# Kernel optimization log

Measured on AMD Instinct MI355X. Metric: run time of the kernel, lower is better.

The kernel has to match this reference:

```python
import jax, jax.numpy as jnp
import numpy as np
from jax import lax

HS, WS = 8, 8  # pattern_size


def setup_inputs() -> dict:
    key = jax.random.key(0)
    k1, k2, k3 = jax.random.split(key, 3)
    B, C, T, H, W = 2, 64, 16, 112, 112
    Cout, K = 64, 3
    x = jax.random.normal(k1, (B, C, T, H, W), dtype=jnp.float32)
    # one independent Conv3d weight/bias per (h, w) phase in the 8x8 pattern
    weight = jax.random.normal(k2, (HS, WS, Cout, C, K, K, K), dtype=jnp.float32) * 0.05
    bias = jax.random.normal(k3, (HS, WS, Cout), dtype=jnp.float32) * 0.05
    return {"x": x, "weight": weight, "bias": bias}


def reference(x, weight, bias):
    hs, ws = HS, WS
    B, C, T, H, W = x.shape
    Cout = weight.shape[2]
    # torch F.pad(x, (hs-1, hs-1, ws-1, ws-1, 1, 1)): W padded by hs-1, H by ws-1, T by 1
    paded = jnp.pad(x, ((0, 0), (0, 0), (1, 1), (ws - 1, ws - 1), (hs - 1, hs - 1)))
    Ho, Wo = H // hs, W // ws  # conv output spatial size per phase: (H-3)//8 + 1 = H//8
    rows = []
    for h in range(hs):
        cols = []
        for w in range(ws):
            sl = paded[:, :, :, h:H + h, w:W + w]  # [B, C, T+2, H, W]
            y = lax.conv_general_dilated(
                sl, weight[h, w],
                window_strides=(1, hs, ws), padding='VALID',
                dimension_numbers=('NCDHW', 'OIDHW', 'NCDHW'))  # [B, Cout, T, Ho, Wo]
            cols.append(y + bias[h, w][None, :, None, None, None])
        rows.append(jnp.stack(cols, 0))
    res = jnp.stack(rows, 0)  # [hs, ws, B, Cout, T, Ho, Wo]
    # out[:, :, :, h + hs*i, w + ws*j] = res[h, w, :, :, :, i, j]
    out = jnp.transpose(res, (2, 3, 4, 5, 0, 6, 1))  # [B, Cout, T, Ho, hs, Wo, ws]
    return out.reshape(B, Cout, T, H, W)
```

## Files before the change

### kernel.cpp

```cpp
#include <hip/hip_runtime.h>
#include <hip/hip_bf16.h>
#include <stdint.h>

typedef __attribute__((ext_vector_type(8))) short short8;
typedef __attribute__((ext_vector_type(4))) float f32x4;

#define WPP_BYTES 14155776ull
#define XPP_BYTES 66355200ull

__device__ __forceinline__ void gl2lds16(const void* g, void* l) {
    __builtin_amdgcn_global_load_lds(
        (const __attribute__((address_space(1))) unsigned int*)g,
        (__attribute__((address_space(3))) unsigned int*)l, 16, 0, 0);
}

__global__ __launch_bounds__(256)
void bzero(uint4* __restrict__ xpp) {
    const uint4 z = {0u, 0u, 0u, 0u};
    const int total = 935936;
    for (int idx = blockIdx.x * 256 + threadIdx.x; idx < total;
         idx += gridDim.x * 256) {
        int u;
        if (idx < 276480) {
            int slab = idx / 2160, off = idx % 2160;
            u = slab * 32400 + off;
        } else if (idx < 534528) {
            int k = idx - 276480;
            int run = k / 144, off = k % 144;
            int slab = run / 14, rho = run % 14 + 1;
            u = slab * 32400 + rho * 2160 + off;
        } else {
            int k = idx - 534528;
            int run = k / 8, off = k % 8;
            int slab = run / 392, r2 = run % 392;
            int rho = r2 / 28 + 1, r3 = r2 % 28;
            int cwo = r3 / 2 + 1, d = (r3 & 1) * 17;
            u = slab * 32400 + rho * 2160 + cwo * 144 + d * 8 + off;
        }
        xpp[u] = z;
    }
}

__global__ __launch_bounds__(512)
void xform_x(const float* __restrict__ xin, __hip_bfloat16* __restrict__ xpp) {
    extern __shared__ __hip_bfloat16 Xl[];
    const int bid = blockIdx.x;
    const int rho = bid % 14, d = (bid / 14) % 16, b = bid / 224;
    const int tid = threadIdx.x;
    for (int f = tid; f < 64 * 8 * 28; f += 512) {
        int ci = f / 224, rem = f % 224;
        int r = rem / 28, c4 = (rem % 28) * 4;
        const float4 v = *(const float4*)&xin[
            ((((size_t)b * 64 + ci) * 16 + d) * 112 + (rho * 8 + r)) * 112 + c4];
        const float vv[4] = {v.x, v.y, v.z, v.w};
#pragma unroll
        for (int u = 0; u < 4; ++u) {
            int c = c4 + u;
            Xl[(r * 112 + c) * 64 + (ci ^ ((c & 7) << 3))] = __float2bfloat16(vv[u]);
        }
    }
    __syncthreads();
    for (int f = tid; f < 896 * 8; f += 512) {
        int pos = f >> 3, j = f & 7;
        int r = pos / 112, c = pos % 112;
        int cw = c & 7, cwo = c >> 3;
        uint4 v = *(const uint4*)&Xl[pos * 64 + ((j * 8) ^ ((c & 7) << 3))];
        size_t dst = (((((size_t)(r * 8 + cw) * 2 + b) * 15 + (rho + 1)) * 15
                       + (cwo + 1)) * 18 + (d + 1)) * 64 + j * 8;
        *(uint4*)(xpp + dst) = v;
    }
}

__global__ __launch_bounds__(256)
void xform_w(const float* __restrict__ wt, __hip_bfloat16* __restrict__ wpp) {
    __shared__ __hip_bfloat16 lw[8 * 27 * 72];
    const int hw = blockIdx.x >> 3, cc = blockIdx.x & 7;
    for (int f = threadIdx.x; f < 8 * 64 * 27; f += 256) {
        int k = f % 27, ci = (f / 27) % 64, co = f / (27 * 64);
        float v = wt[(size_t)hw * 110592 + (size_t)(cc * 8 + co) * 1728 + ci * 27 + k];
        lw[(co * 27 + k) * 72 + ci] = __float2bfloat16(v);
    }
    __syncthreads();
    for (int f = threadIdx.x; f < 27 * 8 * 8; f += 256) {
        int cic = f % 8, co = (f / 8) % 8, k = f / 64;
        uint4 v = *(const uint4*)&lw[(co * 27 + k) * 72 + cic * 8];
        size_t dst = (((size_t)hw * 27 + k) * 64 + (cc * 8 + co)) * 64 + cic * 8;
        *(uint4*)(wpp + dst) = v;
    }
}


__global__ __launch_bounds__(256, 2)
void patgemm(const __hip_bfloat16* __restrict__ xpp,
             const char* __restrict__ wppc,
             const float* __restrict__ bs,
             float* __restrict__ out) {
    extern __shared__ char smem[];
    const char* xppc = (const char*)xpp;
    const int bid = blockIdx.x;
    const int h = bid & 7, w = (bid >> 3) & 7, b = (bid >> 6) & 1, mc = bid >> 7;
    const int hw = h * 8 + w;
    const int tid = threadIdx.x, wv = tid >> 6;
    const int lane = tid & 63, col = lane & 15, quad = lane >> 4;
    const int mg = wv >> 1, ng = wv & 1;

    uint32_t aoff[4];
#pragma unroll
    for (int i = 0; i < 4; ++i) {
        int u = tid + i * 256; if (u > 1007) u = 1007;
        int wo = u / 72, rem = u - wo * 72;
        int d = rem >> 2, qp = rem & 3, q = qp ^ ((d >> 1) & 3);
        aoff[i] = (uint32_t)(wo * 2304 + d * 128 + q * 16);
    }
    uint32_t boff[2];
#pragma unroll
    for (int i = 0; i < 2; ++i) {
        int u = tid + i * 256;
        boff[i] = (uint32_t)((u >> 3) * 128 + (((u & 7) ^ ((u >> 3) & 7)) << 4));
    }
    uint32_t rofs[3];
#pragma unroll
    for (int kd = 0; kd < 3; ++kd) {
        int d = col + kd;
        rofs[kd] = (uint32_t)(d * 64 + ((quad ^ ((d >> 1) & 3)) << 4));
    }
    uint32_t bofsw[2];
#pragma unroll
    for (int hf = 0; hf < 2; ++hf)
        bofsw[hf] = (uint32_t)(col * 128 + (((hf * 4 + quad) ^ (col & 7)) << 4));

    f32x4 acc[7][2];
#pragma unroll
    for (int j = 0; j < 7; ++j)
#pragma unroll
        for (int n = 0; n < 2; ++n) acc[j][n] = (f32x4){0.f, 0.f, 0.f, 0.f};

    const char* wbase = wppc + (size_t)hw * 221184;

    auto lineBase = [&](int p) -> const char* {
        const int kh = (p >= 6) ? 2 : (p >= 3 ? 1 : 0);
        const int kw = p - 3 * kh;
        const int r0 = h + kh - 7, c0 = w + kw - 7;
        return xppc + (size_t)(((((r0 & 7) * 8 + (c0 & 7)) * 2 + b) * 15
                    + ((r0 >> 3) + 1 + mc)) * 15 + ((c0 >> 3) + 1)) * 2304;
    };
    auto STGA = [&](const char* lb, int hf, int buf) {
#pragma unroll
        for (int i = 0; i < 4; ++i)
            gl2lds16(lb + aoff[i] + hf * 64,
                     smem + buf * 16384 + (tid + i * 256) * 16);
    };
    auto STGB = [&](int tap, int slot) {
#pragma unroll
        for (int i = 0; i < 2; ++i)
            gl2lds16(wbase + (size_t)tap * 8192 + boff[i],
                     smem + 32768 + slot * 8192 + (tid + i * 256) * 16);
    };

    const char* lb = lineBase(0);
    STGA(lb, 0, 0);
    STGB(0, 0); STGB(9, 1); STGB(18, 2);
    __syncthreads();

#pragma unroll 1
    for (int p = 0; p < 9; ++p) {
        const int pp = p & 1;
        STGA(lb, 1, 1);
        if (p < 8) {
            const int sb = (1 - pp) * 3;
            STGB(p + 1, sb); STGB(p + 10, sb + 1); STGB(p + 19, sb + 2);
        }
#pragma unroll
        for (int kd = 0; kd < 3; ++kd) {
            const char* Bb = smem + 32768 + (pp * 3 + kd) * 8192;
            short8 bf0 = *(const short8*)(Bb + (ng * 2 + 0) * 2048 + bofsw[0]);
            short8 bf1 = *(const short8*)(Bb + (ng * 2 + 1) * 2048 + bofsw[0]);
#pragma unroll
            for (int j = 0; j < 7; ++j) {
                short8 af = *(const short8*)(smem + (mg * 7 + j) * 1152 + rofs[kd]);
                acc[j][0] = __builtin_amdgcn_mfma_f32_16x16x32_bf16(af, bf0, acc[j][0], 0, 0, 0);
                acc[j][1] = __builtin_amdgcn_mfma_f32_16x16x32_bf16(af, bf1, acc[j][1], 0, 0, 0);
            }
        }
        __syncthreads();
        if (p < 8) { lb = lineBase(p + 1); STGA(lb, 0, 0); }
#pragma unroll
        for (int kd = 0; kd < 3; ++kd) {
            const char* Bb = smem + 32768 + (pp * 3 + kd) * 8192;
            short8 bf0 = *(const short8*)(Bb + (ng * 2 + 0) * 2048 + bofsw[1]);
            short8 bf1 = *(const short8*)(Bb + (ng * 2 + 1) * 2048 + bofsw[1]);
#pragma unroll
            for (int j = 0; j < 7; ++j) {
                short8 af = *(const short8*)(smem + 16384 + (mg * 7 + j) * 1152 + rofs[kd]);
                acc[j][0] = __builtin_amdgcn_mfma_f32_16x16x32_bf16(af, bf0, acc[j][0], 0, 0, 0);
                acc[j][1] = __builtin_amdgcn_mfma_f32_16x16x32_bf16(af, bf1, acc[j][1], 0, 0, 0);
            }
        }
        __syncthreads();
    }

    const float* bsl = bs + hw * 64;
    const int y = 8 * mc + h;
#pragma unroll
    for (int j = 0; j < 7; ++j) {
        const int x = 8 * (mg * 7 + j) + w;
#pragma unroll
        for (int n = 0; n < 2; ++n) {
            const int co = (ng * 2 + n) * 16 + col;
            const float bv = bsl[co];
#pragma unroll
            for (int jj = 0; jj < 4; ++jj) {
                const int t = quad * 4 + jj;
                out[((((size_t)b * 64 + co) * 16 + t) * 112 + y) * 112 + x]
                    = acc[j][n][jj] + bv;
            }
        }
    }
}

#define XL_ROWSTRIDE 116
#define WL_WSTRIDE (17*27)

__global__ __launch_bounds__(256, 3)
void patconv3d_fp32(const float* __restrict__ xin,
                    const float* __restrict__ wt,
                    const float* __restrict__ bs,
                    float* __restrict__ out) {
    __shared__ float Xl[3*3*7*XL_ROWSTRIDE];
    __shared__ float Wl[8*WL_WSTRIDE];
    const int bid = blockIdx.x;
    const int ct = bid & 3, hb = (bid >> 2) & 1, h = (bid >> 3) & 7;
    const int t = (bid >> 6) & 15, b = (bid >> 10) & 1;
    const int tid = threadIdx.x;
    const int xl = tid & 127, cg = tid >> 7;
    const int xr = (xl < 112) ? xl : 111;
    const int wq = xl & 7;
    float acc[8][7];
#pragma unroll
    for (int c = 0; c < 8; ++c)
#pragma unroll
        for (int ho = 0; ho < 7; ++ho) acc[c][ho] = 0.f;
    for (int ci = 0; ci < 64; ++ci) {
        __syncthreads();
        for (int idx = tid; idx < 3 * 3 * 7 * 114; idx += 256) {
            int c = idx % 114, rest = idx / 114;
            int ho = rest % 7; rest /= 7;
            int kh = rest % 3, kd = rest / 3;
            int r = 8 * (hb * 7 + ho) + h + kh - 7;
            int d = t + kd - 1, colx = c - 7;
            float v = 0.f;
            if (r >= 0 && d >= 0 && d < 16 && colx >= 0)
                v = xin[(((size_t)(b * 64 + ci) * 16 + d) * 112 + r) * 112 + colx];
            Xl[((kd * 3 + kh) * 7 + ho) * XL_ROWSTRIDE + c] = v;
        }
        for (int idx = tid; idx < 8 * 16 * 27; idx += 256) {
            int k2 = idx % 27, rest = idx / 27;
            int co_l = rest % 16, wi = rest / 16;
            Wl[wi * WL_WSTRIDE + co_l * 27 + k2] =
                wt[(((size_t)(h * 8 + wi) * 64 + (ct * 16 + co_l)) * 64 + ci) * 27 + k2];
        }
        __syncthreads();
#pragma unroll
        for (int kd = 0; kd < 3; ++kd)
#pragma unroll
            for (int kh = 0; kh < 3; ++kh)
#pragma unroll
                for (int kw = 0; kw < 3; ++kw) {
                    const int k2 = (kd * 3 + kh) * 3 + kw;
                    float xv[7];
#pragma unroll
                    for (int ho = 0; ho < 7; ++ho)
                        xv[ho] = Xl[((kd * 3 + kh) * 7 + ho) * XL_ROWSTRIDE + xr + kw];
                    float wv[8];
#pragma unroll
                    for (int c = 0; c < 8; ++c)
                        wv[c] = Wl[wq * WL_WSTRIDE + (cg * 8 + c) * 27 + k2];
#pragma unroll
                    for (int c = 0; c < 8; ++c)
#pragma unroll
                        for (int ho = 0; ho < 7; ++ho)
                            acc[c][ho] += wv[c] * xv[ho];
                }
    }
    if (xl < 112) {
#pragma unroll
        for (int c = 0; c < 8; ++c) {
            const int co = ct * 16 + cg * 8 + c;
            const float bv = bs[(h * 8 + wq) * 64 + co];
#pragma unroll
            for (int ho = 0; ho < 7; ++ho) {
                const int y = 8 * (hb * 7 + ho) + h;
                out[(((size_t)(b * 64 + co) * 16 + t) * 112 + y) * 112 + xl] = acc[c][ho] + bv;
            }
        }
    }
}

extern "C" void kernel_launch(void* const* d_in, const int* in_sizes, int n_in,
                              void* d_out, int out_size, void* d_ws, size_t ws_size,
                              hipStream_t stream) {
    const float* x  = (const float*)d_in[0];
    const float* wg = (const float*)d_in[1];
    const float* bi = (const float*)d_in[2];
    float* out = (float*)d_out;
    if (ws_size >= WPP_BYTES + XPP_BYTES) {
        __hip_bfloat16* wpp = (__hip_bfloat16*)d_ws;
        __hip_bfloat16* xpp = (__hip_bfloat16*)((char*)d_ws + WPP_BYTES);
        bzero<<<1024, 256, 0, stream>>>((uint4*)xpp);
        xform_x<<<448, 512, 114688, stream>>>(x, xpp);
        xform_w<<<512, 256, 0, stream>>>(wg, wpp);
        patgemm<<<1792, 256, 81920, stream>>>(xpp, (const char*)wpp, bi, out);
    } else {
        patconv3d_fp32<<<2048, 256, 0, stream>>>(x, wg, bi, out);
    }
}
```

Before: 255.8 us.

## Merge prep kernels into one launch; load weights directly to registers

Merges the zero-fill, input transform and weight transform kernels into a single launch, with block-index ranges picking the role, to remove launch gaps. In the GEMM kernel the weight fragments are now loaded from global memory straight into registers each tap instead of being staged in LDS. This shrinks LDS use to 32 KB per block and raises the occupancy hint from 2 to 4 blocks per CU. The cost is more register pressure from twelve held fragments, and weight global loads that are no longer double-buffered and may stall the MFMA loop.

Result: slower. 379.8 us (+48.5%).

```diff
diff --git a/kernel.cpp b/kernel.cpp
--- a/kernel.cpp
+++ b/kernel.cpp
@@ -14,88 +14,87 @@
         (__attribute__((address_space(3))) unsigned int*)l, 16, 0, 0);
 }
 
-__global__ __launch_bounds__(256)
-void bzero(uint4* __restrict__ xpp) {
-    const uint4 z = {0u, 0u, 0u, 0u};
-    const int total = 935936;
-    for (int idx = blockIdx.x * 256 + threadIdx.x; idx < total;
-         idx += gridDim.x * 256) {
-        int u;
-        if (idx < 276480) {
-            int slab = idx / 2160, off = idx % 2160;
-            u = slab * 32400 + off;
-        } else if (idx < 534528) {
-            int k = idx - 276480;
-            int run = k / 144, off = k % 144;
-            int slab = run / 14, rho = run % 14 + 1;
-            u = slab * 32400 + rho * 2160 + off;
-        } else {
-            int k = idx - 534528;
-            int run = k / 8, off = k % 8;
-            int slab = run / 392, r2 = run % 392;
-            int rho = r2 / 28 + 1, r3 = r2 % 28;
-            int cwo = r3 / 2 + 1, d = (r3 & 1) * 17;
-            u = slab * 32400 + rho * 2160 + cwo * 144 + d * 8 + off;
-        }
-        xpp[u] = z;
-    }
-}
-
 __global__ __launch_bounds__(512)
-void xform_x(const float* __restrict__ xin, __hip_bfloat16* __restrict__ xpp) {
-    extern __shared__ __hip_bfloat16 Xl[];
+void prep(const float* __restrict__ xin, const float* __restrict__ wt,
+          __hip_bfloat16* __restrict__ xpp, __hip_bfloat16* __restrict__ wpp) {
+    extern __shared__ char smc[];
     const int bid = blockIdx.x;
-    const int rho = bid % 14, d = (bid / 14) % 16, b = bid / 224;
     const int tid = threadIdx.x;
-    for (int f = tid; f < 64 * 8 * 28; f += 512) {
-        int ci = f / 224, rem = f % 224;
-        int r = rem / 28, c4 = (rem % 28) * 4;
-        const float4 v = *(const float4*)&xin[
-            ((((size_t)b * 64 + ci) * 16 + d) * 112 + (rho * 8 + r)) * 112 + c4];
-        const float vv[4] = {v.x, v.y, v.z, v.w};
-#pragma unroll
-        for (int u = 0; u < 4; ++u) {
-            int c = c4 + u;
-            Xl[(r * 112 + c) * 64 + (ci ^ ((c & 7) << 3))] = __float2bfloat16(vv[u]);
-        }
-    }
-    __syncthreads();
-    for (int f = tid; f < 896 * 8; f += 512) {
-        int pos = f >> 3, j = f & 7;
-        int r = pos / 112, c = pos % 112;
-        int cw = c & 7, cwo = c >> 3;
-        uint4 v = *(const uint4*)&Xl[pos * 64 + ((j * 8) ^ ((c & 7) << 3))];
-        size_t dst = (((((size_t)(r * 8 + cw) * 2 + b) * 15 + (rho + 1)) * 15
-                       + (cwo + 1)) * 18 + (d + 1)) * 64 + j * 8;
-        *(uint4*)(xpp + dst) = v;
-    }
-}
-
-__global__ __launch_bounds__(256)
-void xform_w(const float* __restrict__ wt, __hip_bfloat16* __restrict__ wpp) {
-    __shared__ __hip_bfloat16 lw[8 * 27 * 72];
-    const int hw = blockIdx.x >> 3, cc = blockIdx.x & 7;
-    for (int f = threadIdx.x; f < 8 * 64 * 27; f += 256) {
-        int k = f % 27, ci = (f / 27) % 64, co = f / (27 * 64);
-        float v = wt[(size_t)hw * 110592 + (size_t)(cc * 8 + co) * 1728 + ci * 27 + k];
-        lw[(co * 27 + k) * 72 + ci] = __float2bfloat16(v);
-    }
-    __syncthreads();
-    for (int f = threadIdx.x; f < 27 * 8 * 8; f += 256) {
-        int cic = f % 8, co = (f / 8) % 8, k = f / 64;
-        uint4 v = *(const uint4*)&lw[(co * 27 + k) * 72 + cic * 8];
-        size_t dst = (((size_t)hw * 27 + k) * 64 + (cc * 8 + co)) * 64 + cic * 8;
-        *(uint4*)(wpp + dst) = v;
-    }
-}
-
-
-__global__ __launch_bounds__(256, 2)
+    if (bid < 448) {
+        __hip_bfloat16* Xl = (__hip_bfloat16*)smc;
+        const int rho = bid % 14, d = (bid / 14) % 16, b = bid / 224;
+        for (int f = tid; f < 64 * 8 * 28; f += 512) {
+            int ci = f / 224, rem = f % 224;
+            int r = rem / 28, c4 = (rem % 28) * 4;
+            const float4 v = *(const float4*)&xin[
+                ((((size_t)b * 64 + ci) * 16 + d) * 112 + (rho * 8 + r)) * 112 + c4];
+            const float vv[4] = {v.x, v.y, v.z, v.w};
+#pragma unroll
+            for (int u = 0; u < 4; ++u) {
+                int c = c4 + u;
+                Xl[(r * 112 + c) * 64 + (ci ^ ((c & 7) << 3))] = __float2bfloat16(vv[u]);
+            }
+        }
+        __syncthreads();
+        for (int f = tid; f < 896 * 8; f += 512) {
+            int pos = f >> 3, j = f & 7;
+            int r = pos / 112, c = pos % 112;
+            int cw = c & 7, cwo = c >> 3;
+            uint4 v = *(const uint4*)&Xl[pos * 64 + ((j * 8) ^ ((c & 7) << 3))];
+            size_t dst = (((((size_t)(r * 8 + cw) * 2 + b) * 15 + (rho + 1)) * 15
+                           + (cwo + 1)) * 18 + (d + 1)) * 64 + j * 8;
+            *(uint4*)(xpp + dst) = v;
+        }
+    } else if (bid < 512) {
+        uint4* xp4 = (uint4*)xpp;
+        const uint4 z = {0u, 0u, 0u, 0u};
+        const int total = 935936;
+        for (int idx = (bid - 448) * 512 + tid; idx < total; idx += 64 * 512) {
+            int u;
+            if (idx < 276480) {
+                int slab = idx / 2160, off = idx % 2160;
+                u = slab * 32400 + off;
+            } else if (idx < 534528) {
+                int k = idx - 276480;
+                int run = k / 144, off = k % 144;
+                int slab = run / 14, rho = run % 14 + 1;
+                u = slab * 32400 + rho * 2160 + off;
+            } else {
+                int k = idx - 534528;
+                int run = k / 8, off = k % 8;
+                int slab = run / 392, r2 = run % 392;
+                int rho = r2 / 28 + 1, r3 = r2 % 28;
+                int cwo = r3 / 2 + 1, d = (r3 & 1) * 17;
+                u = slab * 32400 + rho * 2160 + cwo * 144 + d * 8 + off;
+            }
+            xp4[u] = z;
+        }
+    } else {
+        __hip_bfloat16* lw = (__hip_bfloat16*)smc;
+        const int bb = bid - 512;
+        const int hw = bb >> 3, cc = bb & 7;
+        for (int f = tid; f < 8 * 64 * 27; f += 512) {
+            int k = f % 27, ci = (f / 27) % 64, co = f / (27 * 64);
+            float v = wt[(size_t)hw * 110592 + (size_t)(cc * 8 + co) * 1728 + ci * 27 + k];
+            lw[(co * 27 + k) * 72 + ci] = __float2bfloat16(v);
+        }
+        __syncthreads();
+        for (int f = tid; f < 27 * 8 * 8; f += 512) {
+            int cic = f % 8, co = (f / 8) % 8, k = f / 64;
+            uint4 v = *(const uint4*)&lw[(co * 27 + k) * 72 + cic * 8];
+            size_t dst = (((size_t)hw * 27 + k) * 64 + (cc * 8 + co)) * 64 + cic * 8;
+            *(uint4*)(wpp + dst) = v;
+        }
+    }
+}
+
+__global__ __launch_bounds__(256, 4)
 void patgemm(const __hip_bfloat16* __restrict__ xpp,
              const char* __restrict__ wppc,
              const float* __restrict__ bs,
              float* __restrict__ out) {
-    extern __shared__ char smem[];
+    __shared__ uint4 smemv[2048];
+    char* smem = (char*)smemv;
     const char* xppc = (const char*)xpp;
     const int bid = blockIdx.x;
     const int h = bid & 7, w = (bid >> 3) & 7, b = (bid >> 6) & 1, mc = bid >> 7;
@@ -112,30 +111,20 @@
         int d = rem >> 2, qp = rem & 3, q = qp ^ ((d >> 1) & 3);
         aoff[i] = (uint32_t)(wo * 2304 + d * 128 + q * 16);
     }
-    uint32_t boff[2];
-#pragma unroll
-    for (int i = 0; i < 2; ++i) {
-        int u = tid + i * 256;
-        boff[i] = (uint32_t)((u >> 3) * 128 + (((u & 7) ^ ((u >> 3) & 7)) << 4));
-    }
     uint32_t rofs[3];
 #pragma unroll
     for (int kd = 0; kd < 3; ++kd) {
         int d = col + kd;
         rofs[kd] = (uint32_t)(d * 64 + ((quad ^ ((d >> 1) & 3)) << 4));
     }
-    uint32_t bofsw[2];
-#pragma unroll
-    for (int hf = 0; hf < 2; ++hf)
-        bofsw[hf] = (uint32_t)(col * 128 + (((hf * 4 + quad) ^ (col & 7)) << 4));
+    const char* wbase = wppc + (size_t)hw * 221184;
+    const uint32_t bbase = (uint32_t)((ng * 32 + col) * 128 + quad * 16);
 
     f32x4 acc[7][2];
 #pragma unroll
     for (int j = 0; j < 7; ++j)
 #pragma unroll
         for (int n = 0; n < 2; ++n) acc[j][n] = (f32x4){0.f, 0.f, 0.f, 0.f};
-
-    const char* wbase = wppc + (size_t)hw * 221184;
 
     auto lineBase = [&](int p) -> const char* {
         const int kh = (p >= 6) ? 2 : (p >= 3 ? 1 : 0);
@@ -150,50 +139,43 @@
             gl2lds16(lb + aoff[i] + hf * 64,
                      smem + buf * 16384 + (tid + i * 256) * 16);
     };
-    auto STGB = [&](int tap, int slot) {
-#pragma unroll
-        for (int i = 0; i < 2; ++i)
-            gl2lds16(wbase + (size_t)tap * 8192 + boff[i],
-                     smem + 32768 + slot * 8192 + (tid + i * 256) * 16);
-    };
+
+    short8 bfr[12];
 
     const char* lb = lineBase(0);
     STGA(lb, 0, 0);
-    STGB(0, 0); STGB(9, 1); STGB(18, 2);
     __syncthreads();
 
 #pragma unroll 1
     for (int p = 0; p < 9; ++p) {
-        const int pp = p & 1;
+#pragma unroll
+        for (int kd = 0; kd < 3; ++kd)
+#pragma unroll
+            for (int hf = 0; hf < 2; ++hf)
+#pragma unroll
+                for (int n = 0; n < 2; ++n)
+                    bfr[kd * 4 + hf * 2 + n] = *(const short8*)(
+                        wbase + (size_t)(p + 9 * kd) * 8192 + bbase
+                        + n * 2048 + hf * 64);
         STGA(lb, 1, 1);
-        if (p < 8) {
-            const int sb = (1 - pp) * 3;
-            STGB(p + 1, sb); STGB(p + 10, sb + 1); STGB(p + 19, sb + 2);
-        }
 #pragma unroll
         for (int kd = 0; kd < 3; ++kd) {
-            const char* Bb = smem + 32768 + (pp * 3 + kd) * 8192;
-            short8 bf0 = *(const short8*)(Bb + (ng * 2 + 0) * 2048 + bofsw[0]);
-            short8 bf1 = *(const short8*)(Bb + (ng * 2 + 1) * 2048 + bofsw[0]);
 #pragma unroll
             for (int j = 0; j < 7; ++j) {
                 short8 af = *(const short8*)(smem + (mg * 7 + j) * 1152 + rofs[kd]);
-                acc[j][0] = __builtin_amdgcn_mfma_f32_16x16x32_bf16(af, bf0, acc[j][0], 0, 0, 0);
-                acc[j][1] = __builtin_amdgcn_mfma_f32_16x16x32_bf16(af, bf1, acc[j][1], 0, 0, 0);
+                acc[j][0] = __builtin_amdgcn_mfma_f32_16x16x32_bf16(af, bfr[kd * 4 + 0], acc[j][0], 0, 0, 0);
+                acc[j][1] = __builtin_amdgcn_mfma_f32_16x16x32_bf16(af, bfr[kd * 4 + 1], acc[j][1], 0, 0, 0);
             }
         }
         __syncthreads();
         if (p < 8) { lb = lineBase(p + 1); STGA(lb, 0, 0); }
 #pragma unroll
         for (int kd = 0; kd < 3; ++kd) {
-            const char* Bb = smem + 32768 + (pp * 3 + kd) * 8192;
-            short8 bf0 = *(const short8*)(Bb + (ng * 2 + 0) * 2048 + bofsw[1]);
-            short8 bf1 = *(const short8*)(Bb + (ng * 2 + 1) * 2048 + bofsw[1]);
 #pragma unroll
             for (int j = 0; j < 7; ++j) {
                 short8 af = *(const short8*)(smem + 16384 + (mg * 7 + j) * 1152 + rofs[kd]);
-                acc[j][0] = __builtin_amdgcn_mfma_f32_16x16x32_bf16(af, bf0, acc[j][0], 0, 0, 0);
-                acc[j][1] = __builtin_amdgcn_mfma_f32_16x16x32_bf16(af, bf1, acc[j][1], 0, 0, 0);
+                acc[j][0] = __builtin_amdgcn_mfma_f32_16x16x32_bf16(af, bfr[kd * 4 + 2], acc[j][0], 0, 0, 0);
+                acc[j][1] = __builtin_amdgcn_mfma_f32_16x16x32_bf16(af, bfr[kd * 4 + 3], acc[j][1], 0, 0, 0);
             }
         }
         __syncthreads();
@@ -306,10 +288,8 @@
     if (ws_size >= WPP_BYTES + XPP_BYTES) {
         __hip_bfloat16* wpp = (__hip_bfloat16*)d_ws;
         __hip_bfloat16* xpp = (__hip_bfloat16*)((char*)d_ws + WPP_BYTES);
-        bzero<<<1024, 256, 0, stream>>>((uint4*)xpp);
-        xform_x<<<448, 512, 114688, stream>>>(x, xpp);
-        xform_w<<<512, 256, 0, stream>>>(wg, wpp);
-        patgemm<<<1792, 256, 81920, stream>>>(xpp, (const char*)wpp, bi, out);
+        prep<<<1024, 512, 114688, stream>>>(x, wg, xpp, wpp);
+        patgemm<<<1792, 256, 0, stream>>>(xpp, (const char*)wpp, bi, out);
     } else {
         patconv3d_fp32<<<2048, 256, 0, stream>>>(x, wg, bi, out);
     }
```
